# Kernel optimization log

Hardware: AMD Instinct MI355X
Metric: run time of the kernel (lower is better)

Reference implementation:

```python
import jax, jax.numpy as jnp
import numpy as np

B, H, S, D = 2, 16, 2048, 64

def setup_inputs() -> dict:
    key = jax.random.key(0)
    kq, kk, kv = jax.random.split(key, 3)
    q = jax.random.normal(kq, (B, H, S, D), dtype=jnp.float32)
    k = jax.random.normal(kk, (B, H, S, D), dtype=jnp.float32)
    v = jax.random.normal(kv, (B, H, S, D), dtype=jnp.float32)
    return {"q": q, "k": k, "v": v}

def reference(q, k, v):
    scale = q.shape[-1] ** -0.5
    # sim: [b, h, i, j]
    sim = jnp.einsum('bhid,bhjd->bhij', q, k) * scale
    attn = jax.nn.softmax(sim, axis=-1)
    out = jnp.einsum('bhij,bhjd->bhid', attn, v)
    return out
```

## Files before the change

### kernel.cpp

```cpp
#include <hip/hip_runtime.h>

typedef _Float16 f16;
typedef f16 f16x2 __attribute__((ext_vector_type(2)));
typedef f16 f16x4 __attribute__((ext_vector_type(4)));
typedef f16 f16x8 __attribute__((ext_vector_type(8)));
typedef float f32x4 __attribute__((ext_vector_type(4)));

static constexpr int S_LEN  = 2048;
static constexpr int D_DIM  = 64;
static constexpr int NTILE  = 64;
static constexpr float SCALE_LOG2E = 0.1803368801111204f;

#define MFMA32(a,b,c) __builtin_amdgcn_mfma_f32_16x16x32_f16((a),(b),(c),0,0,0)
#define MFMA16(a,b,c) __builtin_amdgcn_mfma_f32_16x16x16f16((a),(b),(c),0,0,0)

__global__ __launch_bounds__(256)
void prepack(const float* __restrict__ kg, const float* __restrict__ vg,
             f16* __restrict__ kp, f16* __restrict__ vp) {
  int b = blockIdx.x;
  const bool isV = (b >= 1024);
  if (isV) b -= 1024;
  const int head = b >> 5;
  const int tile = b & 31;
  const int t = threadIdx.x;
  const size_t base = ((size_t)head * S_LEN + (size_t)tile * NTILE) * D_DIM;

  if (!isV) {
    const float* src = kg + base;
    f16* dst = kp + base;
#pragma unroll
    for (int e = 0; e < 2; ++e) {
      const int ch = e * 256 + t;
      const int j = ch >> 3, c = ch & 7;
      const float* s = src + (size_t)ch * 8;
      float4 a0 = *(const float4*)s;
      float4 a1 = *(const float4*)(s + 4);
      f16x8 o;
      o[0] = (f16)a0.x; o[1] = (f16)a0.y; o[2] = (f16)a0.z; o[3] = (f16)a0.w;
      o[4] = (f16)a1.x; o[5] = (f16)a1.y; o[6] = (f16)a1.z; o[7] = (f16)a1.w;
      const int cK   = (j >> 4) * 2 + (c >> 2);
      const int lanei = (c & 3) * 16 + (j & 15);
      *(f16x8*)(dst + (cK * 64 + lanei) * 8) = o;
    }
  } else {
    __shared__ float ldsv[64 * 68];
    const float* src = vg + base;
#pragma unroll
    for (int i = 0; i < 4; ++i) {
      const int row = t >> 2, col = (t & 3) * 16 + i * 4;
      *(float4*)&ldsv[row * 68 + col] = *(const float4*)(src + row * 64 + col);
    }
    __syncthreads();
    f16* dst = vp + base;
#pragma unroll
    for (int e = 0; e < 2; ++e) {
      const int idx = e * 256 + t;
      const int d = idx >> 3, cl = idx & 7;
      f16x8 o;
#pragma unroll
      for (int s = 0; s < 8; ++s) {
        const int j = (cl & 1) * 32 + (s >> 2) * 16 + (cl >> 1) * 4 + (s & 3);
        o[s] = (f16)ldsv[j * 68 + d];
      }
      const int cV    = (d >> 4) * 2 + (cl & 1);
      const int lanei = (cl >> 1) * 16 + (d & 15);
      *(f16x8*)(dst + (cV * 64 + lanei) * 8) = o;
    }
  }
}

__global__ __launch_bounds__(256, 2)
void attn_pp(const float* __restrict__ qg, const f16* __restrict__ kp,
             const f16* __restrict__ vp, float* __restrict__ og) {
  const int xcd  = blockIdx.x & 7;
  const int slot = blockIdx.x >> 3;
  const int bh   = xcd * 4 + (slot >> 4);
  const int qt   = slot & 15;
  const size_t hbase = (size_t)bh * S_LEN * D_DIM;
  const float* qh = qg + hbase;
  const f16*   kh = kp + hbase;
  const f16*   vh = vp + hbase;
  float*       oh = og + hbase;

  const int tid  = threadIdx.x;
  const int wave = tid >> 6;
  const int lane = tid & 63;
  const int L    = lane & 15;
  const int quad = lane >> 4;

  f16x8 qf[2][2];
  const int qrow0 = qt * 128 + wave * 32;
#pragma unroll
  for (int qs = 0; qs < 2; ++qs)
#pragma unroll
    for (int kc = 0; kc < 2; ++kc) {
      const float* src = qh + (size_t)(qrow0 + qs * 16 + L) * D_DIM + kc * 32 + quad * 8;
      float4 x0 = *(const float4*)src;
      float4 x1 = *(const float4*)(src + 4);
      f16x8 t;
      t[0] = (f16)(x0.x * SCALE_LOG2E); t[1] = (f16)(x0.y * SCALE_LOG2E);
      t[2] = (f16)(x0.z * SCALE_LOG2E); t[3] = (f16)(x0.w * SCALE_LOG2E);
      t[4] = (f16)(x1.x * SCALE_LOG2E); t[5] = (f16)(x1.y * SCALE_LOG2E);
      t[6] = (f16)(x1.z * SCALE_LOG2E); t[7] = (f16)(x1.w * SCALE_LOG2E);
      qf[qs][kc] = t;
    }

  f32x4 oacc[2][4];
#pragma unroll
  for (int qs = 0; qs < 2; ++qs)
#pragma unroll
    for (int dt = 0; dt < 4; ++dt) oacc[qs][dt] = (f32x4){0.f, 0.f, 0.f, 0.f};
  float lsum[2] = {0.f, 0.f};

  f16x8 kf[8], vf[8];
#define LOADK(t_)                                                          \
  do {                                                                     \
    const f16* p = kh + (size_t)(t_) * 4096 + lane * 8;                    \
    _Pragma("unroll")                                                      \
    for (int c = 0; c < 8; ++c) kf[c] = *(const f16x8*)(p + c * 512);      \
  } while (0)
#define LOADV(t_)                                                          \
  do {                                                                     \
    const f16* p = vh + (size_t)(t_) * 4096 + lane * 8;                    \
    _Pragma("unroll")                                                      \
    for (int c = 0; c < 8; ++c) vf[c] = *(const f16x8*)(p + c * 512);      \
  } while (0)

  LOADK(0);
  LOADV(0);

  constexpr int NT = S_LEN / NTILE;
  for (int kt = 0; kt < NT; ++kt) {
    f32x4 sfr[2][4];
#pragma unroll
    for (int qs = 0; qs < 2; ++qs)
#pragma unroll
      for (int jt = 0; jt < 4; ++jt) sfr[qs][jt] = (f32x4){0.f, 0.f, 0.f, 0.f};
#pragma unroll
    for (int jt = 0; jt < 4; ++jt)
#pragma unroll
      for (int kc = 0; kc < 2; ++kc) {
        const f16x8 af = kf[jt * 2 + kc];
        sfr[0][jt] = MFMA32(af, qf[0][kc], sfr[0][jt]);
        sfr[1][jt] = MFMA32(af, qf[1][kc], sfr[1][jt]);
      }

    if (kt + 1 < NT) LOADK(kt + 1);

    f16x4 pf[2][4];
#pragma unroll
    for (int qs = 0; qs < 2; ++qs)
#pragma unroll
      for (int jt = 0; jt < 4; ++jt) {
#pragma unroll
        for (int r = 0; r < 4; ++r)
          pf[qs][jt][r] = (f16)__builtin_amdgcn_exp2f(sfr[qs][jt][r]);
#if __has_builtin(__builtin_amdgcn_fdot2)
        const f16x2 one2 = {(f16)1.f, (f16)1.f};
        f16x2 plo = {pf[qs][jt][0], pf[qs][jt][1]};
        f16x2 phi = {pf[qs][jt][2], pf[qs][jt][3]};
        lsum[qs] = __builtin_amdgcn_fdot2(plo, one2, lsum[qs], false);
        lsum[qs] = __builtin_amdgcn_fdot2(phi, one2, lsum[qs], false);
#else
#pragma unroll
        for (int r = 0; r < 4; ++r) lsum[qs] += (float)pf[qs][jt][r];
#endif
      }

#pragma unroll
    for (int jtp = 0; jtp < 2; ++jtp)
#pragma unroll
      for (int dt = 0; dt < 4; ++dt) {
        const f16x8 vv = vf[dt * 2 + jtp];
        f16x4 vlo = {vv[0], vv[1], vv[2], vv[3]};
        f16x4 vhi = {vv[4], vv[5], vv[6], vv[7]};
        oacc[0][dt] = MFMA16(pf[0][jtp * 2],     vlo, oacc[0][dt]);
        oacc[0][dt] = MFMA16(pf[0][jtp * 2 + 1], vhi, oacc[0][dt]);
        oacc[1][dt] = MFMA16(pf[1][jtp * 2],     vlo, oacc[1][dt]);
        oacc[1][dt] = MFMA16(pf[1][jtp * 2 + 1], vhi, oacc[1][dt]);
      }

    if (kt + 1 < NT) LOADV(kt + 1);
  }
#undef LOADK
#undef LOADV

#pragma unroll
  for (int qs = 0; qs < 2; ++qs) {
    float l = lsum[qs];
    l += __shfl_xor(l, 16);
    l += __shfl_xor(l, 32);
#pragma unroll
    for (int r = 0; r < 4; ++r) {
      const float inv = 1.0f / __shfl(l, quad * 4 + r);
      float* dst = oh + (size_t)(qrow0 + qs * 16 + quad * 4 + r) * D_DIM + L;
#pragma unroll
      for (int dt = 0; dt < 4; ++dt)
        dst[dt * 16] = oacc[qs][dt][r] * inv;
    }
  }
}

static constexpr int MBLOCK = 128;
static constexpr int KST = 72;
static constexpr int VST = 72;
static constexpr float FB_SCALE_LOG2E = 0.1803368801111204f;
static constexpr float FB_SHIFT = 4.0f;

__global__ __launch_bounds__(256, 2)
void attn_fwd_fb(const float* __restrict__ qg, const float* __restrict__ kg,
                 const float* __restrict__ vg, float* __restrict__ og) {
  const int xcd  = blockIdx.x & 7;
  const int slot = blockIdx.x >> 3;
  const int bh   = xcd * 4 + (slot >> 4);
  const int qt   = slot & 15;
  const size_t hbase = (size_t)bh * S_LEN * D_DIM;
  const float* qh = qg + hbase;
  const float* kh = kg + hbase;
  const float* vh = vg + hbase;
  float*       oh = og + hbase;

  const int tid  = threadIdx.x;
  const int wave = tid >> 6;
  const int lane = tid & 63;
  const int L    = lane & 15;
  const int quad = lane >> 4;
  const int lhalf = L >> 3;

  __shared__ f16 Ks[2][NTILE * KST];
  __shared__ f16 Vt[2][D_DIM * VST];

  f16x8 qf[2][2];
  const int qrow0 = qt * MBLOCK + wave * 32;
#pragma unroll
  for (int qs = 0; qs < 2; ++qs)
#pragma unroll
    for (int kc = 0; kc < 2; ++kc) {
      const float* src = qh + (size_t)(qrow0 + qs * 16 + L) * D_DIM + kc * 32 + quad * 8;
      float4 x0 = *(const float4*)src;
      float4 x1 = *(const float4*)(src + 4);
      f16x8 t;
      t[0] = (f16)x0.x; t[1] = (f16)x0.y; t[2] = (f16)x0.z; t[3] = (f16)x0.w;
      t[4] = (f16)x1.x; t[5] = (f16)x1.y; t[6] = (f16)x1.z; t[7] = (f16)x1.w;
      qf[qs][kc] = t;
    }

  f32x4 oacc[2][4];
#pragma unroll
  for (int qs = 0; qs < 2; ++qs)
#pragma unroll
    for (int dt = 0; dt < 4; ++dt) oacc[qs][dt] = (f32x4){0.f, 0.f, 0.f, 0.f};
  float lsum[2] = {0.f, 0.f};

  const int sj  = tid >> 2, sc  = tid & 3;
  const int jd  = tid >> 4, dcc = tid & 15;
  const int vpos = ((jd & 3) * 4 + (jd >> 2)) * 4;
  const int xorv = (dcc >> 1) << 3;
  const float* kstage = kh + (size_t)sj * D_DIM + sc * 4;
  const float* vstage = vh + (size_t)(jd * 4) * D_DIM + dcc * 4;

  float4 kreg[4], vreg[4];
#pragma unroll
  for (int i = 0; i < 4; ++i) {
    kreg[i] = *(const float4*)(kstage + i * 16);
    vreg[i] = *(const float4*)(vstage + (size_t)i * D_DIM);
  }
#pragma unroll
  for (int i = 0; i < 4; ++i) {
    f16x4 t;
    t[0] = (f16)kreg[i].x; t[1] = (f16)kreg[i].y;
    t[2] = (f16)kreg[i].z; t[3] = (f16)kreg[i].w;
    *(f16x4*)&Ks[0][sj * KST + i * 16 + sc * 4] = t;
  }
  {
    const float* vr = reinterpret_cast<const float*>(vreg);
#pragma unroll
    for (int c = 0; c < 4; ++c) {
      f16x4 t;
      t[0] = (f16)vr[0 * 4 + c]; t[1] = (f16)vr[1 * 4 + c];
      t[2] = (f16)vr[2 * 4 + c]; t[3] = (f16)vr[3 * 4 + c];
      *(f16x4*)&Vt[0][(dcc * 4 + c) * VST + (vpos ^ xorv)] = t;
    }
  }
#pragma unroll
  for (int i = 0; i < 4; ++i) {
    kreg[i] = *(const float4*)(kstage + (size_t)1 * NTILE * D_DIM + i * 16);
    vreg[i] = *(const float4*)(vstage + (size_t)1 * NTILE * D_DIM + (size_t)i * D_DIM);
  }
  __syncthreads();

  constexpr int NT = S_LEN / NTILE;
  for (int kt = 0; kt < NT; ++kt) {
    const int cur = kt & 1;
    const int nxt = cur ^ 1;

    f32x4 sfr[2][4];
#pragma unroll
    for (int qs = 0; qs < 2; ++qs)
#pragma unroll
      for (int jt = 0; jt < 4; ++jt) sfr[qs][jt] = (f32x4){0.f, 0.f, 0.f, 0.f};
#pragma unroll
    for (int jt = 0; jt < 4; ++jt)
#pragma unroll
      for (int kc = 0; kc < 2; ++kc) {
        f16x8 af = *(const f16x8*)&Ks[cur][(jt * 16 + L) * KST + kc * 32 + quad * 8];
        sfr[0][jt] = MFMA32(af, qf[0][kc], sfr[0][jt]);
        sfr[1][jt] = MFMA32(af, qf[1][kc], sfr[1][jt]);
      }

    if (kt + 1 < NT) {
#pragma unroll
      for (int i = 0; i < 4; ++i) {
        f16x4 t;
        t[0] = (f16)kreg[i].x; t[1] = (f16)kreg[i].y;
        t[2] = (f16)kreg[i].z; t[3] = (f16)kreg[i].w;
        *(f16x4*)&Ks[nxt][sj * KST + i * 16 + sc * 4] = t;
      }
      const float* vr = reinterpret_cast<const float*>(vreg);
#pragma unroll
      for (int c = 0; c < 4; ++c) {
        f16x4 t;
        t[0] = (f16)vr[0 * 4 + c]; t[1] = (f16)vr[1 * 4 + c];
        t[2] = (f16)vr[2 * 4 + c]; t[3] = (f16)vr[3 * 4 + c];
        *(f16x4*)&Vt[nxt][(dcc * 4 + c) * VST + (vpos ^ xorv)] = t;
      }
    }
    if (kt + 2 < NT) {
      const float* kpp = kstage + (size_t)(kt + 2) * NTILE * D_DIM;
      const float* vpp = vstage + (size_t)(kt + 2) * NTILE * D_DIM;
#pragma unroll
      for (int i = 0; i < 4; ++i) {
        kreg[i] = *(const float4*)(kpp + i * 16);
        vreg[i] = *(const float4*)(vpp + (size_t)i * D_DIM);
      }
    }

    f16x4 pf[2][4];
#pragma unroll
    for (int qs = 0; qs < 2; ++qs)
#pragma unroll
      for (int jt = 0; jt < 4; ++jt) {
#pragma unroll
        for (int r = 0; r < 4; ++r) {
          const float p = __builtin_amdgcn_exp2f(
              __builtin_fmaf(sfr[qs][jt][r], FB_SCALE_LOG2E, -FB_SHIFT));
          lsum[qs] += p;
          pf[qs][jt][r] = (f16)p;
        }
      }

#pragma unroll
    for (int jtp = 0; jtp < 2; ++jtp)
#pragma unroll
      for (int dt = 0; dt < 4; ++dt) {
        const int xorr = ((2 * dt + lhalf) & 7) << 3;
        f16x8 vf = *(const f16x8*)&Vt[cur][(dt * 16 + L) * VST +
                                          ((quad * 16 + jtp * 8) ^ xorr)];
        f16x4 vlo = {vf[0], vf[1], vf[2], vf[3]};
        f16x4 vhi = {vf[4], vf[5], vf[6], vf[7]};
        oacc[0][dt] = MFMA16(pf[0][jtp * 2],     vlo, oacc[0][dt]);
        oacc[0][dt] = MFMA16(pf[0][jtp * 2 + 1], vhi, oacc[0][dt]);
        oacc[1][dt] = MFMA16(pf[1][jtp * 2],     vlo, oacc[1][dt]);
        oacc[1][dt] = MFMA16(pf[1][jtp * 2 + 1], vhi, oacc[1][dt]);
      }

    __syncthreads();
  }

#pragma unroll
  for (int qs = 0; qs < 2; ++qs) {
    float l = lsum[qs];
    l += __shfl_xor(l, 16);
    l += __shfl_xor(l, 32);
#pragma unroll
    for (int r = 0; r < 4; ++r) {
      const float inv = 1.0f / __shfl(l, quad * 4 + r);
      float* dst = oh + (size_t)(qrow0 + qs * 16 + quad * 4 + r) * D_DIM + L;
#pragma unroll
      for (int dt = 0; dt < 4; ++dt)
        dst[dt * 16] = oacc[qs][dt][r] * inv;
    }
  }
}

extern "C" void kernel_launch(void* const* d_in, const int* in_sizes, int n_in,
                              void* d_out, int out_size, void* d_ws, size_t ws_size,
                              hipStream_t stream) {
  const float* q = (const float*)d_in[0];
  const float* k = (const float*)d_in[1];
  const float* v = (const float*)d_in[2];
  float* o = (float*)d_out;

  const size_t kv_elems = (size_t)32 * S_LEN * D_DIM;
  const size_t need = 2 * kv_elems * sizeof(f16);

  if (ws_size >= need && d_ws != nullptr) {
    f16* kp = (f16*)d_ws;
    f16* vp = kp + kv_elems;
    prepack<<<dim3(2048), dim3(256), 0, stream>>>(k, v, kp, vp);
    attn_pp<<<dim3(512), dim3(256), 0, stream>>>(q, kp, vp, o);
  } else {
    attn_fwd_fb<<<dim3(512), dim3(256), 0, stream>>>(q, k, v, o);
  }
}
```

Baseline: 135.3 us.

## Double-buffer V fragments and vectorize V prepack LDS reads

```diff
diff --git a/kernel.cpp b/kernel.cpp
--- a/kernel.cpp
+++ b/kernel.cpp
@@ -38,7 +38,7 @@
       f16x8 o;
       o[0] = (f16)a0.x; o[1] = (f16)a0.y; o[2] = (f16)a0.z; o[3] = (f16)a0.w;
       o[4] = (f16)a1.x; o[5] = (f16)a1.y; o[6] = (f16)a1.z; o[7] = (f16)a1.w;
-      const int cK   = (j >> 4) * 2 + (c >> 2);
+      const int cK    = (j >> 4) * 2 + (c >> 2);
       const int lanei = (c & 3) * 16 + (j & 15);
       *(f16x8*)(dst + (cK * 64 + lanei) * 8) = o;
     }
@@ -52,19 +52,23 @@
     }
     __syncthreads();
     f16* dst = vp + base;
-#pragma unroll
-    for (int e = 0; e < 2; ++e) {
-      const int idx = e * 256 + t;
-      const int d = idx >> 3, cl = idx & 7;
-      f16x8 o;
-#pragma unroll
-      for (int s = 0; s < 8; ++s) {
-        const int j = (cl & 1) * 32 + (s >> 2) * 16 + (cl >> 1) * 4 + (s & 3);
-        o[s] = (f16)ldsv[j * 68 + d];
-      }
-      const int cV    = (d >> 4) * 2 + (cl & 1);
-      const int lanei = (cl >> 1) * 16 + (d & 15);
-      *(f16x8*)(dst + (cV * 64 + lanei) * 8) = o;
+    const int d0 = (t >> 3) * 2;
+    const int cl = t & 7;
+    f16x8 o0, o1;
+#pragma unroll
+    for (int s = 0; s < 8; ++s) {
+      const int j = (cl & 1) * 32 + (s >> 2) * 16 + ((cl >> 1) & 3) * 4 + (s & 3);
+      const float2 v2 = *(const float2*)&ldsv[j * 68 + d0];
+      o0[s] = (f16)v2.x; o1[s] = (f16)v2.y;
+    }
+    {
+      const int cV0 = (d0 >> 4) * 2 + (cl & 1);
+      const int li0 = (cl >> 1) * 16 + (d0 & 15);
+      *(f16x8*)(dst + (cV0 * 64 + li0) * 8) = o0;
+      const int d1 = d0 + 1;
+      const int cV1 = (d1 >> 4) * 2 + (cl & 1);
+      const int li1 = (cl >> 1) * 16 + (d1 & 15);
+      *(f16x8*)(dst + (cV1 * 64 + li1) * 8) = o1;
     }
   }
 }
@@ -112,26 +116,21 @@
     for (int dt = 0; dt < 4; ++dt) oacc[qs][dt] = (f32x4){0.f, 0.f, 0.f, 0.f};
   float lsum[2] = {0.f, 0.f};
 
-  f16x8 kf[8], vf[8];
+  f16x8 kf[8], vfA[8], vfB[8];
 #define LOADK(t_)                                                          \
   do {                                                                     \
     const f16* p = kh + (size_t)(t_) * 4096 + lane * 8;                    \
     _Pragma("unroll")                                                      \
     for (int c = 0; c < 8; ++c) kf[c] = *(const f16x8*)(p + c * 512);      \
   } while (0)
-#define LOADV(t_)                                                          \
+#define LOADV(buf, t_)                                                     \
   do {                                                                     \
     const f16* p = vh + (size_t)(t_) * 4096 + lane * 8;                    \
     _Pragma("unroll")                                                      \
-    for (int c = 0; c < 8; ++c) vf[c] = *(const f16x8*)(p + c * 512);      \
+    for (int c = 0; c < 8; ++c) buf[c] = *(const f16x8*)(p + c * 512);     \
   } while (0)
 
-  LOADK(0);
-  LOADV(0);
-
-  constexpr int NT = S_LEN / NTILE;
-  for (int kt = 0; kt < NT; ++kt) {
-    f32x4 sfr[2][4];
+  auto qk_phase = [&](f32x4 (&sfr)[2][4]) {
 #pragma unroll
     for (int qs = 0; qs < 2; ++qs)
 #pragma unroll
@@ -144,10 +143,8 @@
         sfr[0][jt] = MFMA32(af, qf[0][kc], sfr[0][jt]);
         sfr[1][jt] = MFMA32(af, qf[1][kc], sfr[1][jt]);
       }
-
-    if (kt + 1 < NT) LOADK(kt + 1);
-
-    f16x4 pf[2][4];
+  };
+  auto sm_phase = [&](f32x4 (&sfr)[2][4], f16x4 (&pf)[2][4]) {
 #pragma unroll
     for (int qs = 0; qs < 2; ++qs)
 #pragma unroll
@@ -166,7 +163,8 @@
         for (int r = 0; r < 4; ++r) lsum[qs] += (float)pf[qs][jt][r];
 #endif
       }
-
+  };
+  auto pv_phase = [&](f16x4 (&pf)[2][4], f16x8 (&vf)[8]) {
 #pragma unroll
     for (int jtp = 0; jtp < 2; ++jtp)
 #pragma unroll
@@ -179,8 +177,32 @@
         oacc[1][dt] = MFMA16(pf[1][jtp * 2],     vlo, oacc[1][dt]);
         oacc[1][dt] = MFMA16(pf[1][jtp * 2 + 1], vhi, oacc[1][dt]);
       }
-
-    if (kt + 1 < NT) LOADV(kt + 1);
+  };
+
+  constexpr int NT = S_LEN / NTILE;
+  LOADK(0);
+  LOADV(vfA, 0);
+
+  for (int p = 0; p < NT / 2; ++p) {
+    const int t1 = 2 * p + 1;
+    {
+      f32x4 sfr[2][4]; f16x4 pf[2][4];
+      qk_phase(sfr);
+      LOADK(t1);
+      LOADV(vfB, t1);
+      sm_phase(sfr, pf);
+      pv_phase(pf, vfA);
+    }
+    {
+      f32x4 sfr[2][4]; f16x4 pf[2][4];
+      qk_phase(sfr);
+      if (t1 + 1 < NT) {
+        LOADK(t1 + 1);
+        LOADV(vfA, t1 + 1);
+      }
+      sm_phase(sfr, pf);
+      pv_phase(pf, vfB);
+    }
   }
 #undef LOADK
 #undef LOADV
```

Measured after the change: 141.7 us. +4.7%, slower.
